# Kernel optimization log

Measured on AMD Instinct MI355X. Metric: run time of the kernel, lower is better.

Reference implementation:

```python
import jax, jax.numpy as jnp
import numpy as np

SCALE_PARAM = 1e-09

def setup_inputs() -> dict:
    key = jax.random.key(0)
    keypoints = jax.random.normal(key, (32, 8192, 128), dtype=jnp.float32)
    return {"keypoints": keypoints}

def reference(keypoints):
    # Original: sep_loss = sum_i mean_{b,j,d} (x[b,i,d] - x[b,j,d])^2
    #         = (1/(B*N*D)) * sum_{b,d} sum_{i,j} (x_bid - x_bjd)^2
    # Pairwise identity per (b,d): sum_{i,j}(xi-xj)^2 = 2*N*sum_i xi^2 - 2*(sum_i xi)^2
    B, N, D = keypoints.shape
    sum_sq = jnp.sum(keypoints * keypoints)            # sum_{b,i,d} x^2
    s = jnp.sum(keypoints, axis=1)                      # [B, D], sum over keypoints
    total = 2.0 * N * sum_sq - 2.0 * jnp.sum(s * s)
    sep_loss = total / (B * N * D)
    return jnp.exp(-SCALE_PARAM * sep_loss)
```

## Files before the change

### kernel.cpp

```cpp
#include <hip/hip_runtime.h>
#include <math.h>

#define B 32
#define N 8192
#define D 128
#define SCALE_PARAM 1e-9f

__global__ __launch_bounds__(256) void partial_kernel(
    const float* __restrict__ x,
    float* __restrict__ s_out,
    float* __restrict__ ssq_out)
{
    __shared__ float lds_s[8][D];
    __shared__ float lds_ssq[4];

    const int t  = threadIdx.x;
    const int d4 = t & 31;
    const int rg = t >> 5;

    const long long row_base = (long long)blockIdx.x * 128;
    const int b = (int)(row_base >> 13);

    const float4* __restrict__ x4 = (const float4*)x;

    float4 acc = make_float4(0.f, 0.f, 0.f, 0.f);
    float ssq = 0.f;

    #pragma unroll
    for (int it = 0; it < 16; ++it) {
        const long long row = row_base + it * 8 + rg;
        const float4 v = x4[row * (D / 4) + d4];
        acc.x += v.x; acc.y += v.y; acc.z += v.z; acc.w += v.w;
        ssq += v.x * v.x + v.y * v.y + v.z * v.z + v.w * v.w;
    }

    lds_s[rg][d4 * 4 + 0] = acc.x;
    lds_s[rg][d4 * 4 + 1] = acc.y;
    lds_s[rg][d4 * 4 + 2] = acc.z;
    lds_s[rg][d4 * 4 + 3] = acc.w;

    #pragma unroll
    for (int off = 32; off > 0; off >>= 1)
        ssq += __shfl_down(ssq, off);
    if ((t & 63) == 0) lds_ssq[t >> 6] = ssq;

    __syncthreads();

    if (t < D) {
        float sd = 0.f;
        #pragma unroll
        for (int r = 0; r < 8; ++r) sd += lds_s[r][t];
        atomicAdd(&s_out[b * D + t], sd);
    }
    if (t == 0) {
        atomicAdd(ssq_out, lds_ssq[0] + lds_ssq[1] + lds_ssq[2] + lds_ssq[3]);
    }
}

__global__ __launch_bounds__(256) void finalize_kernel(
    const float* __restrict__ s,
    const float* __restrict__ ssq,
    float* __restrict__ out)
{
    __shared__ float lds[4];
    const int t = threadIdx.x;

    float acc = 0.f;
    for (int i = t; i < B * D; i += 256) {
        const float v = s[i];
        acc += v * v;
    }
    #pragma unroll
    for (int off = 32; off > 0; off >>= 1)
        acc += __shfl_down(acc, off);
    if ((t & 63) == 0) lds[t >> 6] = acc;
    __syncthreads();

    if (t == 0) {
        const float sum_s2 = lds[0] + lds[1] + lds[2] + lds[3];
        const float sum_sq = ssq[0];
        const float total  = 2.0f * (float)N * sum_sq - 2.0f * sum_s2;
        const float sep    = total / ((float)B * (float)N * (float)D);
        out[0] = expf(-SCALE_PARAM * sep);
    }
}

extern "C" void kernel_launch(void* const* d_in, const int* in_sizes, int n_in,
                              void* d_out, int out_size, void* d_ws, size_t ws_size,
                              hipStream_t stream) {
    const float* x = (const float*)d_in[0];
    float* out = (float*)d_out;

    float* s_ws   = (float*)d_ws;
    float* ssq_ws = s_ws + B * D;

    hipMemsetAsync(d_ws, 0, (B * D + 1) * sizeof(float), stream);

    const int total_rows = B * N;
    const int blocks = total_rows / 128;
    partial_kernel<<<blocks, 256, 0, stream>>>(x, s_ws, ssq_ws);
    finalize_kernel<<<1, 256, 0, stream>>>(s_ws, ssq_ws, out);
}
```

Measured before the change: 195.7 us.

## Replace atomics and memset with per-block partials reduced in a 1024-thread finalize

Each block now writes its per-column sums and sum of squares to its own slot in workspace instead of issuing atomicAdds, which also removes the hipMemsetAsync launch. The finalize kernel grows to 1024 threads and reduces the 2048x128 partials per batch before squaring. Loads become nontemporal vector loads, and LDS stores are vectorised. The tradeoff is that finalize now reads about 1 MB of partials serially in a single block, which may cost more than the removed atomics.

New measurement: 186.1 us. 1.05x faster.

```diff
diff --git a/kernel.cpp b/kernel.cpp
--- a/kernel.cpp
+++ b/kernel.cpp
@@ -6,38 +6,38 @@
 #define D 128
 #define SCALE_PARAM 1e-9f
 
+#define ROWS_PER_BLOCK 128
+#define NBLOCKS ((B * N) / ROWS_PER_BLOCK)
+
+typedef float __attribute__((ext_vector_type(4))) f32x4;
+
 __global__ __launch_bounds__(256) void partial_kernel(
     const float* __restrict__ x,
-    float* __restrict__ s_out,
-    float* __restrict__ ssq_out)
+    float* __restrict__ P,
+    float* __restrict__ SS)
 {
-    __shared__ float lds_s[8][D];
+    __shared__ f32x4 lds_s4[8][32];
     __shared__ float lds_ssq[4];
 
     const int t  = threadIdx.x;
     const int d4 = t & 31;
     const int rg = t >> 5;
 
-    const long long row_base = (long long)blockIdx.x * 128;
-    const int b = (int)(row_base >> 13);
+    const int row_base = blockIdx.x * ROWS_PER_BLOCK;
+    const f32x4* __restrict__ x4 = (const f32x4*)x;
 
-    const float4* __restrict__ x4 = (const float4*)x;
-
-    float4 acc = make_float4(0.f, 0.f, 0.f, 0.f);
+    f32x4 acc = {0.f, 0.f, 0.f, 0.f};
     float ssq = 0.f;
 
     #pragma unroll
     for (int it = 0; it < 16; ++it) {
-        const long long row = row_base + it * 8 + rg;
-        const float4 v = x4[row * (D / 4) + d4];
-        acc.x += v.x; acc.y += v.y; acc.z += v.z; acc.w += v.w;
+        const int row = row_base + it * 8 + rg;
+        const f32x4 v = __builtin_nontemporal_load(&x4[row * (D / 4) + d4]);
+        acc += v;
         ssq += v.x * v.x + v.y * v.y + v.z * v.z + v.w * v.w;
     }
 
-    lds_s[rg][d4 * 4 + 0] = acc.x;
-    lds_s[rg][d4 * 4 + 1] = acc.y;
-    lds_s[rg][d4 * 4 + 2] = acc.z;
-    lds_s[rg][d4 * 4 + 3] = acc.w;
+    lds_s4[rg][d4] = acc;
 
     #pragma unroll
     for (int off = 32; off > 0; off >>= 1)
@@ -47,40 +47,58 @@
     __syncthreads();
 
     if (t < D) {
+        const float* lds_f = (const float*)lds_s4;
         float sd = 0.f;
         #pragma unroll
-        for (int r = 0; r < 8; ++r) sd += lds_s[r][t];
-        atomicAdd(&s_out[b * D + t], sd);
+        for (int r = 0; r < 8; ++r) sd += lds_f[r * D + t];
+        P[blockIdx.x * D + t] = sd;
     }
     if (t == 0) {
-        atomicAdd(ssq_out, lds_ssq[0] + lds_ssq[1] + lds_ssq[2] + lds_ssq[3]);
+        SS[blockIdx.x] = lds_ssq[0] + lds_ssq[1] + lds_ssq[2] + lds_ssq[3];
     }
 }
 
-__global__ __launch_bounds__(256) void finalize_kernel(
-    const float* __restrict__ s,
-    const float* __restrict__ ssq,
+#define BLOCKS_PER_B (N / ROWS_PER_BLOCK)
+__global__ __launch_bounds__(1024) void finalize_kernel(
+    const float* __restrict__ P,
+    const float* __restrict__ SS,
     float* __restrict__ out)
 {
-    __shared__ float lds[4];
+    __shared__ float l1[16], l2[16];
     const int t = threadIdx.x;
 
-    float acc = 0.f;
-    for (int i = t; i < B * D; i += 256) {
-        const float v = s[i];
-        acc += v * v;
+    float acc_s2 = 0.f;
+    #pragma unroll
+    for (int pp = 0; pp < 4; ++pp) {
+        const int p = t + pp * 1024;
+        const int b = p >> 7;
+        const int d = p & (D - 1);
+        float s = 0.f;
+        #pragma unroll 8
+        for (int k = 0; k < BLOCKS_PER_B; ++k)
+            s += P[(b * BLOCKS_PER_B + k) * D + d];
+        acc_s2 += s * s;
     }
+
+    float acc_ssq = 0.f;
     #pragma unroll
-    for (int off = 32; off > 0; off >>= 1)
-        acc += __shfl_down(acc, off);
-    if ((t & 63) == 0) lds[t >> 6] = acc;
+    for (int pp = 0; pp < 2; ++pp)
+        acc_ssq += SS[t + pp * 1024];
+
+    #pragma unroll
+    for (int off = 32; off > 0; off >>= 1) {
+        acc_s2  += __shfl_down(acc_s2, off);
+        acc_ssq += __shfl_down(acc_ssq, off);
+    }
+    if ((t & 63) == 0) { l1[t >> 6] = acc_s2; l2[t >> 6] = acc_ssq; }
     __syncthreads();
 
     if (t == 0) {
-        const float sum_s2 = lds[0] + lds[1] + lds[2] + lds[3];
-        const float sum_sq = ssq[0];
-        const float total  = 2.0f * (float)N * sum_sq - 2.0f * sum_s2;
-        const float sep    = total / ((float)B * (float)N * (float)D);
+        float sum_s2 = 0.f, sum_sq = 0.f;
+        #pragma unroll
+        for (int w = 0; w < 16; ++w) { sum_s2 += l1[w]; sum_sq += l2[w]; }
+        const float total = 2.0f * (float)N * sum_sq - 2.0f * sum_s2;
+        const float sep   = total / ((float)B * (float)N * (float)D);
         out[0] = expf(-SCALE_PARAM * sep);
     }
 }
@@ -91,13 +109,9 @@
     const float* x = (const float*)d_in[0];
     float* out = (float*)d_out;
 
-    float* s_ws   = (float*)d_ws;
-    float* ssq_ws = s_ws + B * D;
+    float* P  = (float*)d_ws;
+    float* SS = P + NBLOCKS * D;
 
-    hipMemsetAsync(d_ws, 0, (B * D + 1) * sizeof(float), stream);
-
-    const int total_rows = B * N;
-    const int blocks = total_rows / 128;
-    partial_kernel<<<blocks, 256, 0, stream>>>(x, s_ws, ssq_ws);
-    finalize_kernel<<<1, 256, 0, stream>>>(s_ws, ssq_ws, out);
+    partial_kernel<<<NBLOCKS, 256, 0, stream>>>(x, P, SS);
+    finalize_kernel<<<1, 1024, 0, stream>>>(P, SS, out);
 }
```
